# Kernel tuning notes

Measured on AMD Instinct MI355X. Metric: run time of the kernel, lower is better.

## Reference

```python
import jax, jax.numpy as jnp
import numpy as np

NUM_NODES = 100000
EMBED_DIM = 256
NUM_EDGES = 16384
TOTAL = 524288  # total flattened hyperedge membership entries


def setup_inputs() -> dict:
    key = jax.random.key(0)
    k1, k2, k3 = jax.random.split(key, 3)
    node_embeddings = jax.random.normal(k1, (NUM_NODES, EMBED_DIM), dtype=jnp.float32)
    node_indices = jax.random.randint(k2, (TOTAL,), 0, NUM_NODES, dtype=jnp.int64)
    segment_ids = jnp.sort(jax.random.randint(k3, (TOTAL,), 0, NUM_EDGES, dtype=jnp.int64))
    return {"node_embeddings": node_embeddings, "node_indices": node_indices, "segment_ids": segment_ids}


def reference(node_embeddings, node_indices, segment_ids):
    # Gather member-node embeddings: [TOTAL, D]
    gathered = node_embeddings[node_indices]
    # Segmented sum over hyperedges: [NUM_EDGES, D]
    seg_sum = jax.ops.segment_sum(gathered, segment_ids, num_segments=NUM_EDGES)
    # Per-hyperedge member counts for the mean; guard empty segments.
    counts = jax.ops.segment_sum(jnp.ones((gathered.shape[0],), dtype=gathered.dtype),
                                 segment_ids, num_segments=NUM_EDGES)
    counts = jnp.maximum(counts, 1.0)
    return seg_sum / counts[:, None]
```

## Files before the change

kernel.cpp:

```cpp
#include <hip/hip_runtime.h>
#include <hip/hip_fp16.h>


#define EMBED_DIM 256
#define NUM_EDGES 16384
#define TOTAL_MEM 524288
#define NUM_NODES 100000

#define TAB16_BYTES ((size_t)NUM_NODES * EMBED_DIM * 2)
#define BOUNDS_BYTES ((size_t)(NUM_EDGES + 1) * sizeof(int))

__global__ __launch_bounds__(256) void convert_f32_to_f16_kernel(
    const float4* __restrict__ in,
    uint4*        __restrict__ out)
{
    const int j = blockIdx.x * blockDim.x + threadIdx.x;
    const int n_out = NUM_NODES * (EMBED_DIM / 8);
    if (j >= n_out) return;
    float4 a = in[2 * j];
    float4 b = in[2 * j + 1];
    __half2 h0 = __floats2half2_rn(a.x, a.y);
    __half2 h1 = __floats2half2_rn(a.z, a.w);
    __half2 h2 = __floats2half2_rn(b.x, b.y);
    __half2 h3 = __floats2half2_rn(b.z, b.w);
    uint4 o;
    o.x = *reinterpret_cast<unsigned int*>(&h0);
    o.y = *reinterpret_cast<unsigned int*>(&h1);
    o.z = *reinterpret_cast<unsigned int*>(&h2);
    o.w = *reinterpret_cast<unsigned int*>(&h3);
    out[j] = o;
}

__global__ __launch_bounds__(256) void seg_bounds_kernel(
    const int* __restrict__ seg_ids,
    int*       __restrict__ seg_start)
{
    const int i = blockIdx.x * blockDim.x + threadIdx.x;
    if (i >= TOTAL_MEM) return;
    const int cur  = seg_ids[i];
    const int prev = (i == 0) ? -1 : seg_ids[i - 1];
    for (int s = prev + 1; s <= cur; ++s) seg_start[s] = i;
    if (i == TOTAL_MEM - 1) {
        for (int s = cur + 1; s <= NUM_EDGES; ++s) seg_start[s] = TOTAL_MEM;
    }
}

__global__ __launch_bounds__(256) void hyperedge_agg_f16_kernel(
    const uint2* __restrict__ tab,
    const int*   __restrict__ node_idx,
    const int*   __restrict__ seg_start,
    float*       __restrict__ out)
{
    const int wave = threadIdx.x >> 6;
    const int lane = threadIdx.x & 63;
    const int seg  = blockIdx.x * 4 + wave;
    if (seg >= NUM_EDGES) return;

    const int start = seg_start[seg];
    const int end   = seg_start[seg + 1];

    float4 acc = make_float4(0.f, 0.f, 0.f, 0.f);

    int i = start;
    while (i < end) {
        const int batch = min(end - i, 64);
        const int my = (lane < batch) ? node_idx[i + lane] : 0;

        for (int j = 0; j < batch; j += 8) {
            const int m = min(batch - j, 8);
            uint2 v[8];
            #pragma unroll
            for (int t = 0; t < 8; ++t)
                if (t < m) {
                    const int n = __shfl(my, j + t);
                    v[t] = tab[(size_t)n * (EMBED_DIM / 4) + lane];
                }
            #pragma unroll
            for (int t = 0; t < 8; ++t)
                if (t < m) {
                    __half2 h0 = *reinterpret_cast<__half2*>(&v[t].x);
                    __half2 h1 = *reinterpret_cast<__half2*>(&v[t].y);
                    float2 f0 = __half22float2(h0);
                    float2 f1 = __half22float2(h1);
                    acc.x += f0.x; acc.y += f0.y;
                    acc.z += f1.x; acc.w += f1.y;
                }
        }
        i += batch;
    }

    const float cnt = (end > start) ? (float)(end - start) : 1.0f;
    acc.x /= cnt; acc.y /= cnt; acc.z /= cnt; acc.w /= cnt;

    ((float4*)(out + (size_t)seg * EMBED_DIM))[lane] = acc;
}


__global__ __launch_bounds__(256) void hyperedge_agg_kernel(
    const float* __restrict__ emb,
    const int*   __restrict__ node_idx,
    const int*   __restrict__ seg_start,
    float*       __restrict__ out)
{
    const int wave = threadIdx.x >> 6;
    const int lane = threadIdx.x & 63;
    const int seg  = blockIdx.x * 4 + wave;
    if (seg >= NUM_EDGES) return;

    const int start = seg_start[seg];
    const int end   = seg_start[seg + 1];

    float4 acc = make_float4(0.f, 0.f, 0.f, 0.f);
    int i = start;
    while (i < end) {
        const int batch = min(end - i, 64);
        const int my = (lane < batch) ? node_idx[i + lane] : 0;
        for (int j = 0; j < batch; j += 8) {
            const int m = min(batch - j, 8);
            float4 v[8];
            #pragma unroll
            for (int t = 0; t < 8; ++t)
                if (t < m) {
                    const int n = __shfl(my, j + t);
                    v[t] = ((const float4*)(emb + (size_t)n * EMBED_DIM))[lane];
                }
            #pragma unroll
            for (int t = 0; t < 8; ++t)
                if (t < m) {
                    acc.x += v[t].x; acc.y += v[t].y;
                    acc.z += v[t].z; acc.w += v[t].w;
                }
        }
        i += batch;
    }
    const float cnt = (end > start) ? (float)(end - start) : 1.0f;
    acc.x /= cnt; acc.y /= cnt; acc.z /= cnt; acc.w /= cnt;
    ((float4*)(out + (size_t)seg * EMBED_DIM))[lane] = acc;
}

__global__ __launch_bounds__(256) void hyperedge_agg_bsearch_kernel(
    const float* __restrict__ emb,
    const int*   __restrict__ node_idx,
    const int*   __restrict__ seg_ids,
    float*       __restrict__ out)
{
    const int wave = threadIdx.x >> 6;
    const int lane = threadIdx.x & 63;
    const int seg  = blockIdx.x * 4 + wave;
    if (seg >= NUM_EDGES) return;

    int lo = 0, hi = TOTAL_MEM;
    while (lo < hi) {
        int mid = (lo + hi) >> 1;
        if (seg_ids[mid] < seg) lo = mid + 1; else hi = mid;
    }
    const int start = lo;
    hi = TOTAL_MEM;
    while (lo < hi) {
        int mid = (lo + hi) >> 1;
        if (seg_ids[mid] < seg + 1) lo = mid + 1; else hi = mid;
    }
    const int end = lo;

    float4 acc = make_float4(0.f, 0.f, 0.f, 0.f);
    for (int i = start; i < end; ++i) {
        const int n = node_idx[i];
        float4 v = ((const float4*)(emb + (size_t)n * EMBED_DIM))[lane];
        acc.x += v.x; acc.y += v.y; acc.z += v.z; acc.w += v.w;
    }
    const float cnt = (end > start) ? (float)(end - start) : 1.0f;
    acc.x /= cnt; acc.y /= cnt; acc.z /= cnt; acc.w /= cnt;
    ((float4*)(out + (size_t)seg * EMBED_DIM))[lane] = acc;
}

extern "C" void kernel_launch(void* const* d_in, const int* in_sizes, int n_in,
                              void* d_out, int out_size, void* d_ws, size_t ws_size,
                              hipStream_t stream) {
    const float* emb      = (const float*)d_in[0];
    const int*   node_idx = (const int*)d_in[1];
    const int*   seg_ids  = (const int*)d_in[2];
    float*       out      = (float*)d_out;

    if (ws_size >= TAB16_BYTES + BOUNDS_BYTES) {
        uint4* tab16     = (uint4*)d_ws;
        int*   seg_start = (int*)((char*)d_ws + TAB16_BYTES);

        const int n_out4 = NUM_NODES * (EMBED_DIM / 8);
        convert_f32_to_f16_kernel<<<(n_out4 + 255) / 256, 256, 0, stream>>>(
            (const float4*)emb, tab16);
        seg_bounds_kernel<<<(TOTAL_MEM + 255) / 256, 256, 0, stream>>>(seg_ids, seg_start);
        hyperedge_agg_f16_kernel<<<NUM_EDGES / 4, 256, 0, stream>>>(
            (const uint2*)tab16, node_idx, seg_start, out);
    } else if (ws_size >= BOUNDS_BYTES) {
        int* seg_start = (int*)d_ws;
        seg_bounds_kernel<<<(TOTAL_MEM + 255) / 256, 256, 0, stream>>>(seg_ids, seg_start);
        hyperedge_agg_kernel<<<NUM_EDGES / 4, 256, 0, stream>>>(emb, node_idx, seg_start, out);
    } else {
        hyperedge_agg_bsearch_kernel<<<NUM_EDGES / 4, 256, 0, stream>>>(emb, node_idx, seg_ids, out);
    }
}
```

Baseline: 208.5 us.

## Slice fp16 table by feature columns and fuse prep kernels

Fuses the fp32-to-fp16 conversion and segment-bounds computation into one launch. Stores the fp16 table in 8 column slices, each 32 features wide and laid out contiguously per slice. The aggregation kernel now runs 8 blocks per segment group, one per slice, so each slice's working set (about 6.4 MB) is more likely to stay in cache. In each wave, 8 members are gathered at once at 64 B each, then reduced with cross-lane shuffles. This trades more blocks and repeated index loads per slice for better cache locality of the gathers and one fewer kernel launch.

```diff
diff --git a/kernel.cpp b/kernel.cpp
--- a/kernel.cpp
+++ b/kernel.cpp
@@ -10,30 +10,109 @@
 #define TAB16_BYTES ((size_t)NUM_NODES * EMBED_DIM * 2)
 #define BOUNDS_BYTES ((size_t)(NUM_EDGES + 1) * sizeof(int))
 
-__global__ __launch_bounds__(256) void convert_f32_to_f16_kernel(
-    const float4* __restrict__ in,
-    uint4*        __restrict__ out)
-{
-    const int j = blockIdx.x * blockDim.x + threadIdx.x;
-    const int n_out = NUM_NODES * (EMBED_DIM / 8);
-    if (j >= n_out) return;
-    float4 a = in[2 * j];
-    float4 b = in[2 * j + 1];
-    __half2 h0 = __floats2half2_rn(a.x, a.y);
-    __half2 h1 = __floats2half2_rn(a.z, a.w);
-    __half2 h2 = __floats2half2_rn(b.x, b.y);
-    __half2 h3 = __floats2half2_rn(b.z, b.w);
-    uint4 o;
-    o.x = *reinterpret_cast<unsigned int*>(&h0);
-    o.y = *reinterpret_cast<unsigned int*>(&h1);
-    o.z = *reinterpret_cast<unsigned int*>(&h2);
-    o.w = *reinterpret_cast<unsigned int*>(&h3);
-    out[j] = o;
-}
+#define CONV_BLOCKS   12500
+#define BOUNDS_BLOCKS 2048
+
+__global__ __launch_bounds__(256) void prep_kernel(
+    const float4* __restrict__ emb4,
+    uint4*        __restrict__ tab,
+    const int*    __restrict__ seg_ids,
+    int*          __restrict__ seg_start)
+{
+    const int b = blockIdx.x;
+    if (b < CONV_BLOCKS) {
+        const int u  = b * 256 + threadIdx.x;
+        const int n  = u >> 5;
+        const int d8 = u & 31;
+        float4 a = emb4[(size_t)n * 64 + d8 * 2];
+        float4 c = emb4[(size_t)n * 64 + d8 * 2 + 1];
+        __half2 h0 = __floats2half2_rn(a.x, a.y);
+        __half2 h1 = __floats2half2_rn(a.z, a.w);
+        __half2 h2 = __floats2half2_rn(c.x, c.y);
+        __half2 h3 = __floats2half2_rn(c.z, c.w);
+        uint4 o;
+        o.x = *reinterpret_cast<unsigned int*>(&h0);
+        o.y = *reinterpret_cast<unsigned int*>(&h1);
+        o.z = *reinterpret_cast<unsigned int*>(&h2);
+        o.w = *reinterpret_cast<unsigned int*>(&h3);
+        const int p = d8 >> 2;
+        const int q = d8 & 3;
+        tab[((size_t)p * NUM_NODES + n) * 4 + q] = o;
+    } else {
+        const int i = (b - CONV_BLOCKS) * 256 + threadIdx.x;
+        if (i >= TOTAL_MEM) return;
+        const int cur  = seg_ids[i];
+        const int prev = (i == 0) ? -1 : seg_ids[i - 1];
+        for (int s = prev + 1; s <= cur; ++s) seg_start[s] = i;
+        if (i == TOTAL_MEM - 1) {
+            for (int s = cur + 1; s <= NUM_EDGES; ++s) seg_start[s] = TOTAL_MEM;
+        }
+    }
+}
+
+__global__ __launch_bounds__(256) void agg_sliced_kernel(
+    const uint2* __restrict__ tab,
+    const int*   __restrict__ node_idx,
+    const int*   __restrict__ seg_start,
+    float*       __restrict__ out)
+{
+    const int wave  = threadIdx.x >> 6;
+    const int lane  = threadIdx.x & 63;
+    const int slice = blockIdx.x & 7;
+    const int seg   = (blockIdx.x >> 3) * 4 + wave;
+    if (seg >= NUM_EDGES) return;
+
+    const int start = seg_start[seg];
+    const int end   = seg_start[seg + 1];
+
+    const uint2* sub = tab + (size_t)slice * NUM_NODES * 8;
+    const int m   = lane >> 3;
+    const int d8r = lane & 7;
+
+    float4 acc = make_float4(0.f, 0.f, 0.f, 0.f);
+
+    for (int i = start; i < end; i += 64) {
+        const int batch = min(end - i, 64);
+        const int my = (lane < batch) ? node_idx[i + lane] : 0;
+
+        uint2 v[8];
+        #pragma unroll
+        for (int g = 0; g < 8; ++g) {
+            v[g] = make_uint2(0u, 0u);
+            const int msel = g * 8 + m;
+            const int n = __shfl(my, msel);
+            if (msel < batch)
+                v[g] = sub[(size_t)n * 8 + d8r];
+        }
+        #pragma unroll
+        for (int g = 0; g < 8; ++g) {
+            __half2 h0 = *reinterpret_cast<__half2*>(&v[g].x);
+            __half2 h1 = *reinterpret_cast<__half2*>(&v[g].y);
+            float2 f0 = __half22float2(h0);
+            float2 f1 = __half22float2(h1);
+            acc.x += f0.x; acc.y += f0.y;
+            acc.z += f1.x; acc.w += f1.y;
+        }
+    }
+
+    #pragma unroll
+    for (int s = 8; s <= 32; s <<= 1) {
+        acc.x += __shfl_xor(acc.x, s);
+        acc.y += __shfl_xor(acc.y, s);
+        acc.z += __shfl_xor(acc.z, s);
+        acc.w += __shfl_xor(acc.w, s);
+    }
+
+    const float cnt = (end > start) ? (float)(end - start) : 1.0f;
+    acc.x /= cnt; acc.y /= cnt; acc.z /= cnt; acc.w /= cnt;
+
+    if (lane < 8)
+        ((float4*)(out + (size_t)seg * EMBED_DIM + slice * 32))[lane] = acc;
+}
+
 
 __global__ __launch_bounds__(256) void seg_bounds_kernel(
-    const int* __restrict__ seg_ids,
-    int*       __restrict__ seg_start)
+    const int* __restrict__ seg_ids, int* __restrict__ seg_start)
 {
     const int i = blockIdx.x * blockDim.x + threadIdx.x;
     if (i >= TOTAL_MEM) return;
@@ -45,57 +124,6 @@
     }
 }
 
-__global__ __launch_bounds__(256) void hyperedge_agg_f16_kernel(
-    const uint2* __restrict__ tab,
-    const int*   __restrict__ node_idx,
-    const int*   __restrict__ seg_start,
-    float*       __restrict__ out)
-{
-    const int wave = threadIdx.x >> 6;
-    const int lane = threadIdx.x & 63;
-    const int seg  = blockIdx.x * 4 + wave;
-    if (seg >= NUM_EDGES) return;
-
-    const int start = seg_start[seg];
-    const int end   = seg_start[seg + 1];
-
-    float4 acc = make_float4(0.f, 0.f, 0.f, 0.f);
-
-    int i = start;
-    while (i < end) {
-        const int batch = min(end - i, 64);
-        const int my = (lane < batch) ? node_idx[i + lane] : 0;
-
-        for (int j = 0; j < batch; j += 8) {
-            const int m = min(batch - j, 8);
-            uint2 v[8];
-            #pragma unroll
-            for (int t = 0; t < 8; ++t)
-                if (t < m) {
-                    const int n = __shfl(my, j + t);
-                    v[t] = tab[(size_t)n * (EMBED_DIM / 4) + lane];
-                }
-            #pragma unroll
-            for (int t = 0; t < 8; ++t)
-                if (t < m) {
-                    __half2 h0 = *reinterpret_cast<__half2*>(&v[t].x);
-                    __half2 h1 = *reinterpret_cast<__half2*>(&v[t].y);
-                    float2 f0 = __half22float2(h0);
-                    float2 f1 = __half22float2(h1);
-                    acc.x += f0.x; acc.y += f0.y;
-                    acc.z += f1.x; acc.w += f1.y;
-                }
-        }
-        i += batch;
-    }
-
-    const float cnt = (end > start) ? (float)(end - start) : 1.0f;
-    acc.x /= cnt; acc.y /= cnt; acc.z /= cnt; acc.w /= cnt;
-
-    ((float4*)(out + (size_t)seg * EMBED_DIM))[lane] = acc;
-}
-
-
 __global__ __launch_bounds__(256) void hyperedge_agg_kernel(
     const float* __restrict__ emb,
     const int*   __restrict__ node_idx,
@@ -116,17 +144,17 @@
         const int batch = min(end - i, 64);
         const int my = (lane < batch) ? node_idx[i + lane] : 0;
         for (int j = 0; j < batch; j += 8) {
-            const int m = min(batch - j, 8);
+            const int mm = min(batch - j, 8);
             float4 v[8];
             #pragma unroll
             for (int t = 0; t < 8; ++t)
-                if (t < m) {
+                if (t < mm) {
                     const int n = __shfl(my, j + t);
                     v[t] = ((const float4*)(emb + (size_t)n * EMBED_DIM))[lane];
                 }
             #pragma unroll
             for (int t = 0; t < 8; ++t)
-                if (t < m) {
+                if (t < mm) {
                     acc.x += v[t].x; acc.y += v[t].y;
                     acc.z += v[t].z; acc.w += v[t].w;
                 }
@@ -185,11 +213,9 @@
         uint4* tab16     = (uint4*)d_ws;
         int*   seg_start = (int*)((char*)d_ws + TAB16_BYTES);
 
-        const int n_out4 = NUM_NODES * (EMBED_DIM / 8);
-        convert_f32_to_f16_kernel<<<(n_out4 + 255) / 256, 256, 0, stream>>>(
-            (const float4*)emb, tab16);
-        seg_bounds_kernel<<<(TOTAL_MEM + 255) / 256, 256, 0, stream>>>(seg_ids, seg_start);
-        hyperedge_agg_f16_kernel<<<NUM_EDGES / 4, 256, 0, stream>>>(
+        prep_kernel<<<CONV_BLOCKS + BOUNDS_BLOCKS, 256, 0, stream>>>(
+            (const float4*)emb, tab16, seg_ids, seg_start);
+        agg_sliced_kernel<<<(NUM_EDGES / 4) * 8, 256, 0, stream>>>(
             (const uint2*)tab16, node_idx, seg_start, out);
     } else if (ws_size >= BOUNDS_BYTES) {
         int* seg_start = (int*)d_ws;
```

After: 214.5 us. 1.03x slower.
